# Optimization experiments

Hardware: AMD Instinct MI355X
Metric: run time of the kernel (lower is better)

## Reference

```python
import jax, jax.numpy as jnp
import numpy as np

B, C, H, W = 8, 256, 80, 80
NH, NP = 8, 4               # num_heads, num_points
CPH = C // NH               # channels per head


def conv1x1(x, w, b):
    # x: [B,Cin,H,W], w: [Cout,Cin], b: [Cout]
    return jnp.einsum('bchw,oc->bohw', x, w) + b[None, :, None, None]


def grid_sample_bilinear(img, grid):
    # img: [N,C,Hi,Wi], grid: [N,Hg,Wg,2] in [-1,1] (x,y), align_corners=True, zeros padding
    N, Cc, Hi, Wi = img.shape
    Hg, Wg = grid.shape[1], grid.shape[2]
    ix = (grid[..., 0] + 1.0) * 0.5 * (Wi - 1)
    iy = (grid[..., 1] + 1.0) * 0.5 * (Hi - 1)
    x0 = jnp.floor(ix); y0 = jnp.floor(iy)
    x1 = x0 + 1.0;      y1 = y0 + 1.0
    wx1 = ix - x0; wx0 = 1.0 - wx1
    wy1 = iy - y0; wy0 = 1.0 - wy1
    imf = img.reshape(N, Cc, Hi * Wi)

    def gather(xc, yc):
        valid = (xc >= 0) & (xc <= Wi - 1) & (yc >= 0) & (yc <= Hi - 1)
        xi = jnp.clip(xc, 0, Wi - 1).astype(jnp.int32)
        yi = jnp.clip(yc, 0, Hi - 1).astype(jnp.int32)
        idx = (yi * Wi + xi).reshape(N, 1, Hg * Wg)
        v = jnp.take_along_axis(imf, jnp.broadcast_to(idx, (N, Cc, Hg * Wg)), axis=2)
        v = v.reshape(N, Cc, Hg, Wg)
        return v * valid[:, None].astype(img.dtype)

    out = (gather(x0, y0) * (wx0 * wy0)[:, None]
           + gather(x1, y0) * (wx1 * wy0)[:, None]
           + gather(x0, y1) * (wx0 * wy1)[:, None]
           + gather(x1, y1) * (wx1 * wy1)[:, None])
    return out


def setup_inputs() -> dict:
    key = jax.random.key(0)
    ks = jax.random.split(key, 9)
    s = 1.0 / np.sqrt(C)
    x = jax.random.normal(ks[0], (B, C, H, W), dtype=jnp.float32)
    Wv = jax.random.normal(ks[1], (C, C), dtype=jnp.float32) * s
    bv = jnp.zeros((C,), dtype=jnp.float32)
    Woff = jax.random.normal(ks[2], (NH * NP * 2, C), dtype=jnp.float32) * 0.01
    boff = jax.random.normal(ks[3], (NH * NP * 2,), dtype=jnp.float32) * 0.01
    Wa = jax.random.normal(ks[4], (NH * NP, C), dtype=jnp.float32) * 0.01
    ba = jnp.full((NH * NP,), float(np.log(1.0 / NP)), dtype=jnp.float32)
    Wo = jax.random.normal(ks[5], (C, C), dtype=jnp.float32) * s
    bo = jnp.zeros((C,), dtype=jnp.float32)
    return {"x": x, "Wv": Wv, "bv": bv, "Woff": Woff, "boff": boff,
            "Wa": Wa, "ba": ba, "Wo": Wo, "bo": bo}


def reference(x, Wv, bv, Woff, boff, Wa, ba, Wo, bo):
    value = conv1x1(x, Wv, bv)                      # [B,C,H,W]
    offsets = conv1x1(x, Woff, boff)                # [B,NH*NP*2,H,W]
    attn = conv1x1(x, Wa, ba).reshape(B, NH, NP, H, W)
    attn = jax.nn.softmax(attn, axis=2)             # softmax over points

    gy, gx = jnp.meshgrid(jnp.linspace(-1.0, 1.0, H), jnp.linspace(-1.0, 1.0, W), indexing='ij')
    base_grid = jnp.stack((gx, gy), axis=-1)[None, None, None]          # [1,1,1,H,W,2]

    off = offsets.reshape(B, NH, NP, 2, H, W).transpose(0, 1, 2, 4, 5, 3)  # [B,NH,NP,H,W,2]
    grid = (base_grid + off).reshape(B * NH * NP, H, W, 2)

    v = value.reshape(B, NH, CPH, H, W)
    v = jnp.broadcast_to(v[:, :, None], (B, NH, NP, CPH, H, W)).reshape(B * NH * NP, CPH, H, W)

    sampled = grid_sample_bilinear(v, grid).reshape(B, NH, NP, CPH, H, W)
    weighted = (sampled * attn[:, :, :, None]).sum(axis=2)              # [B,NH,CPH,H,W]
    weighted = weighted.reshape(B, C, H, W)
    return conv1x1(weighted, Wo, bo) + x
```

## Files before the change

kernel.cpp:

```cpp
#include <hip/hip_runtime.h>
#include <cstddef>
#include <cstdint>

#define B_    8
#define C_    256
#define Himg  80
#define Wimg  80
#define HW_   6400
#define NH_   8
#define NP_   4
#define MPROJ 352

using bf16x8 = __attribute__((ext_vector_type(8))) short;
using f32x4  = __attribute__((ext_vector_type(4))) float;

__device__ __forceinline__ unsigned short f2bf(float f) {
    union { float f; uint32_t u; } v; v.f = f;
    uint32_t r = v.u + 0x7FFFu + ((v.u >> 16) & 1u);
    return (unsigned short)(r >> 16);
}
__device__ __forceinline__ float bf2f(unsigned short s) {
    union { uint32_t u; float f; } v; v.u = ((uint32_t)s) << 16;
    return v.f;
}

#define GLD16(gsrc, ldst) \
    __builtin_amdgcn_global_load_lds( \
        (const __attribute__((address_space(1))) unsigned int*)(gsrc), \
        (__attribute__((address_space(3))) unsigned int*)(ldst), 16, 0, 0)

__global__ __launch_bounds__(256) void prep_w(
        const float* __restrict__ Wv,  const float* __restrict__ bv,
        const float* __restrict__ Woff, const float* __restrict__ boff,
        const float* __restrict__ Wa,  const float* __restrict__ ba,
        const float* __restrict__ Wo,
        short* __restrict__ WcatBf, short* __restrict__ WoBf,
        float* __restrict__ bcat) {
    int o = blockIdx.x, t = threadIdx.x;
    if (o < 384) {
        const float* src = nullptr; float bias = 0.f;
        if (o < 256)      { src = Wv   + (size_t)o * 256;         bias = bv[o];         }
        else if (o < 320) { src = Woff + (size_t)(o - 256) * 256; bias = boff[o - 256]; }
        else if (o < 352) { src = Wa   + (size_t)(o - 320) * 256; bias = ba[o - 320];   }
        WcatBf[(size_t)o * 256 + t] = src ? (short)f2bf(src[t]) : (short)0;
        if (t == 0) bcat[o] = bias;
    } else {
        int oo = o - 384;
        WoBf[(size_t)oo * 256 + t] = (short)f2bf(Wo[(size_t)oo * 256 + t]);
    }
}

__global__ __launch_bounds__(256) void transpose_x(
        const float* __restrict__ x, short* __restrict__ xT) {
    __shared__ float tile[64][68];
    const int b = blockIdx.z, k0 = blockIdx.y * 64, p0 = blockIdx.x * 64;
    const int t = threadIdx.x;
    const float* xb = x + ((size_t)b * C_ + k0) * HW_ + p0;
    #pragma unroll
    for (int r = 0; r < 4; ++r) {
        int kk = r * 16 + (t >> 4);
        int pp = (t & 15) * 4;
        float4 v = *(const float4*)(xb + (size_t)kk * HW_ + pp);
        *(float4*)&tile[kk][pp] = v;
    }
    __syncthreads();
    const int pp = t >> 2, kc = (t & 3) * 16;
    short tmp[16];
    #pragma unroll
    for (int i = 0; i < 16; ++i) tmp[i] = (short)f2bf(tile[kc + i][pp]);
    short* dst = xT + ((size_t)b * HW_ + p0 + pp) * 256 + k0 + kc;
    *(bf16x8*)dst       = *(bf16x8*)tmp;
    *(bf16x8*)(dst + 8) = *(bf16x8*)(tmp + 8);
}

#define PSTAGE(buf, k0)                                                         \
    _Pragma("unroll")                                                           \
    for (int q = 0; q < 4; ++q) {                                               \
        int i = wid * 4 + q;                                                    \
        int row = i * 8 + (lane >> 3);                                          \
        int sc  = (lane & 7) ^ (row & 7);                                       \
        GLD16(Wb  + (size_t)(o0 + row) * 256 + (k0) + sc * 8,                   \
              &lA[(buf)][i * 512]);                                             \
        GLD16(xTb + (size_t)(p0 + row) * 256 + (k0) + sc * 8,                   \
              &lB[(buf)][i * 512]);                                             \
    }

#define PCOMPUTE(buf)                                                           \
    _Pragma("unroll")                                                           \
    for (int kk = 0; kk < 2; ++kk) {                                            \
        bf16x8 af[4], bfr[4];                                                   \
        _Pragma("unroll")                                                       \
        for (int m = 0; m < 4; ++m) {                                           \
            int row = wo0 + m * 16 + (lane & 15);                               \
            int cph = (kk * 4 + (lane >> 4)) ^ (row & 7);                       \
            af[m] = *(const bf16x8*)&lA[(buf)][row * 64 + cph * 8];             \
        }                                                                       \
        _Pragma("unroll")                                                       \
        for (int nn = 0; nn < 4; ++nn) {                                        \
            int row = wp0 + nn * 16 + (lane & 15);                              \
            int cph = (kk * 4 + (lane >> 4)) ^ (row & 7);                       \
            bfr[nn] = *(const bf16x8*)&lB[(buf)][row * 64 + cph * 8];           \
        }                                                                       \
        _Pragma("unroll")                                                       \
        for (int m = 0; m < 4; ++m)                                             \
            _Pragma("unroll")                                                   \
            for (int nn = 0; nn < 4; ++nn)                                      \
                acc[m][nn] = __builtin_amdgcn_mfma_f32_16x16x32_bf16(           \
                    af[m], bfr[nn], acc[m][nn], 0, 0, 0);                       \
    }

__global__ __launch_bounds__(256) void gemm_proj_mfma(
        const short* __restrict__ Wb, const float* __restrict__ bcat,
        const short* __restrict__ xT,
        short* __restrict__ val, float* __restrict__ meta) {
    __shared__ short lA[2][8192];
    __shared__ short lB[2][8192];
    const int n = blockIdx.x;
    const int w = (n & 7) * 150 + (n >> 3);
    const int b = w / 150;
    const int r150 = w % 150;
    const int o0 = (r150 / 50) * 128;
    const int p0 = (r150 % 50) * 128;
    const int t = threadIdx.x;
    const int wid = t >> 6, lane = t & 63;
    const int wo0 = (wid & 1) * 64, wp0 = (wid >> 1) * 64;
    const short* xTb = xT + (size_t)b * HW_ * 256;
    f32x4 acc[4][4] = {};

    PSTAGE(0, 0)
    __syncthreads();
    #pragma unroll
    for (int kt = 0; kt < 3; ++kt) {
        const int cur = kt & 1;
        PSTAGE(cur ^ 1, (kt + 1) * 64)
        PCOMPUTE(cur)
        __syncthreads();
    }
    PCOMPUTE(1)

    #pragma unroll
    for (int m = 0; m < 4; ++m) {
        int oc = o0 + wo0 + m * 16 + (lane >> 4) * 4;
        if (oc >= MPROJ) continue;
        float4 bias = *(const float4*)(bcat + oc);
        #pragma unroll
        for (int nn = 0; nn < 4; ++nn) {
            int p = p0 + wp0 + nn * 16 + (lane & 15);
            f32x4 a = acc[m][nn];
            float v0 = a[0] + bias.x, v1 = a[1] + bias.y;
            float v2 = a[2] + bias.z, v3 = a[3] + bias.w;
            if (oc < 256) {
                ushort4 u;
                u.x = f2bf(v0); u.y = f2bf(v1); u.z = f2bf(v2); u.w = f2bf(v3);
                *(ushort4*)(val + ((size_t)b * HW_ + p) * 256 + oc) = u;
            } else {
                float4 f; f.x = v0; f.y = v1; f.z = v2; f.w = v3;
                *(float4*)(meta + ((size_t)b * HW_ + p) * 96 + (oc - 256)) = f;
            }
        }
    }
}

__global__ __launch_bounds__(256) void sample_kern(
        const short* __restrict__ val, const float* __restrict__ meta,
        short* __restrict__ wout) {
    const int t = threadIdx.x;
    const int wid = t >> 6, lane = t & 63;
    const int sub = lane >> 5, li = lane & 31;
    const int h = li >> 2, j = li & 3;
    const int orig = blockIdx.x;
    const int b = orig & 7;
    const int p = (orig >> 3) * 8 + wid * 2 + sub;
    const int yy = p / Wimg;
    const int xx = p - yy * Wimg;

    const float* mrow = meta + ((size_t)b * HW_ + p) * 96;
    float4 lg = *(const float4*)(mrow + 64 + h * 4);
    float mx  = fmaxf(fmaxf(lg.x, lg.y), fmaxf(lg.z, lg.w));
    float e0 = __expf(lg.x - mx), e1 = __expf(lg.y - mx);
    float e2 = __expf(lg.z - mx), e3 = __expf(lg.w - mx);
    float inv = 1.f / (e0 + e1 + e2 + e3);
    float wgt[4] = {e0 * inv, e1 * inv, e2 * inv, e3 * inv};

    float4 offA = *(const float4*)(mrow + h * 8);
    float4 offB = *(const float4*)(mrow + h * 8 + 4);
    float ox[4] = {offA.x, offA.z, offB.x, offB.z};
    float oy[4] = {offA.y, offA.w, offB.y, offB.w};

    const short* vb = val + (size_t)b * HW_ * 256 + h * 32 + j * 8;

    float acc[8] = {};
    #pragma unroll
    for (int pt = 0; pt < NP_; ++pt) {
        float ix = (float)xx + ox[pt] * 39.5f;
        float iy = (float)yy + oy[pt] * 39.5f;
        float x0f = floorf(ix), y0f = floorf(iy);
        int   x0  = (int)x0f,   y0  = (int)y0f;
        float wx1 = ix - x0f, wx0 = 1.f - wx1;
        float wy1 = iy - y0f, wy0 = 1.f - wy1;
        int x0c = min(max(x0, 0), Wimg - 1), x1c = min(max(x0 + 1, 0), Wimg - 1);
        int y0c = min(max(y0, 0), Himg - 1), y1c = min(max(y0 + 1, 0), Himg - 1);
        float vx0 = (x0 >= 0 && x0 <= Wimg - 1)         ? wx0 : 0.f;
        float vx1 = (x0 + 1 >= 0 && x0 + 1 <= Wimg - 1) ? wx1 : 0.f;
        float vy0 = (y0 >= 0 && y0 <= Himg - 1)         ? wy0 : 0.f;
        float vy1 = (y0 + 1 >= 0 && y0 + 1 <= Himg - 1) ? wy1 : 0.f;
        bf16x8 u00 = *(const bf16x8*)(vb + (size_t)(y0c * Wimg + x0c) * 256);
        bf16x8 u01 = *(const bf16x8*)(vb + (size_t)(y0c * Wimg + x1c) * 256);
        bf16x8 u10 = *(const bf16x8*)(vb + (size_t)(y1c * Wimg + x0c) * 256);
        bf16x8 u11 = *(const bf16x8*)(vb + (size_t)(y1c * Wimg + x1c) * 256);
        float w00 = vy0 * vx0 * wgt[pt], w01 = vy0 * vx1 * wgt[pt];
        float w10 = vy1 * vx0 * wgt[pt], w11 = vy1 * vx1 * wgt[pt];
        #pragma unroll
        for (int c = 0; c < 8; ++c) {
            acc[c] += w00 * bf2f((unsigned short)u00[c])
                    + w01 * bf2f((unsigned short)u01[c])
                    + w10 * bf2f((unsigned short)u10[c])
                    + w11 * bf2f((unsigned short)u11[c]);
        }
    }
    short tmp[8];
    #pragma unroll
    for (int c = 0; c < 8; ++c) tmp[c] = (short)f2bf(acc[c]);
    *(bf16x8*)(wout + ((size_t)b * HW_ + p) * 256 + h * 32 + j * 8) = *(bf16x8*)tmp;
}

#define OSTAGE(buf, k0)                                                         \
    _Pragma("unroll")                                                           \
    for (int q = 0; q < 2; ++q) {                                               \
        int i = wid * 2 + q;                                                    \
        int row = i * 8 + (lane >> 3);                                          \
        int sc  = (lane & 7) ^ (row & 7);                                       \
        GLD16(Wb + (size_t)(o0 + row) * 256 + (k0) + sc * 8,                    \
              &lA[(buf)][i * 512]);                                             \
    }                                                                           \
    _Pragma("unroll")                                                           \
    for (int q = 0; q < 4; ++q) {                                               \
        int i = wid * 4 + q;                                                    \
        int row = i * 8 + (lane >> 3);                                          \
        int sc  = (lane & 7) ^ (row & 7);                                       \
        GLD16(wgtb + (size_t)(p0 + row) * 256 + (k0) + sc * 8,                  \
              &lB[(buf)][i * 512]);                                             \
    }

#define OCOMPUTE(buf)                                                           \
    _Pragma("unroll")                                                           \
    for (int kk = 0; kk < 2; ++kk) {                                            \
        bf16x8 af[4], bfr[2];                                                   \
        _Pragma("unroll")                                                       \
        for (int m = 0; m < 4; ++m) {                                           \
            int row = m * 16 + (lane & 15);                                     \
            int cph = (kk * 4 + (lane >> 4)) ^ (row & 7);                       \
            af[m] = *(const bf16x8*)&lA[(buf)][row * 64 + cph * 8];             \
        }                                                                       \
        _Pragma("unroll")                                                       \
        for (int nn = 0; nn < 2; ++nn) {                                        \
            int row = wid * 32 + nn * 16 + (lane & 15);                         \
            int cph = (kk * 4 + (lane >> 4)) ^ (row & 7);                       \
            bfr[nn] = *(const bf16x8*)&lB[(buf)][row * 64 + cph * 8];           \
        }                                                                       \
        _Pragma("unroll")                                                       \
        for (int m = 0; m < 4; ++m)                                             \
            _Pragma("unroll")                                                   \
            for (int nn = 0; nn < 2; ++nn)                                      \
                acc[m][nn] = __builtin_amdgcn_mfma_f32_16x16x32_bf16(           \
                    af[m], bfr[nn], acc[m][nn], 0, 0, 0);                       \
    }

__global__ __launch_bounds__(256) void gemm_out_mfma(
        const short* __restrict__ Wb, const float* __restrict__ bo,
        const short* __restrict__ wgt, const float* __restrict__ x,
        float* __restrict__ out) {
    __shared__ short lA[2][4096];
    __shared__ short lB[2][8192];
    const int n = blockIdx.x;
    const int w = (n & 7) * 200 + (n >> 3);
    const int b = w / 200;
    const int r200 = w % 200;
    const int o0 = (r200 / 50) * 64;
    const int p0 = (r200 % 50) * 128;
    const int t = threadIdx.x;
    const int wid = t >> 6, lane = t & 63;
    const short* wgtb = wgt + (size_t)b * HW_ * 256;
    f32x4 acc[4][2] = {};

    OSTAGE(0, 0)
    __syncthreads();
    #pragma unroll
    for (int kt = 0; kt < 3; ++kt) {
        const int cur = kt & 1;
        OSTAGE(cur ^ 1, (kt + 1) * 64)
        OCOMPUTE(cur)
        __syncthreads();
    }
    OCOMPUTE(1)

    #pragma unroll
    for (int m = 0; m < 4; ++m) {
        int oc = o0 + m * 16 + (lane >> 4) * 4;
        float4 bias = *(const float4*)(bo + oc);
        float br[4] = {bias.x, bias.y, bias.z, bias.w};
        #pragma unroll
        for (int nn = 0; nn < 2; ++nn) {
            int p = p0 + wid * 32 + nn * 16 + (lane & 15);
            f32x4 a = acc[m][nn];
            #pragma unroll
            for (int reg = 0; reg < 4; ++reg) {
                size_t ad = ((size_t)b * C_ + oc + reg) * HW_ + p;
                out[ad] = a[reg] + br[reg] + x[ad];
            }
        }
    }
}

extern "C" void kernel_launch(void* const* d_in, const int* in_sizes, int n_in,
                              void* d_out, int out_size, void* d_ws, size_t ws_size,
                              hipStream_t stream) {
    const float* x    = (const float*)d_in[0];
    const float* Wv   = (const float*)d_in[1];
    const float* bv   = (const float*)d_in[2];
    const float* Woff = (const float*)d_in[3];
    const float* boff = (const float*)d_in[4];
    const float* Wa   = (const float*)d_in[5];
    const float* ba   = (const float*)d_in[6];
    const float* Wo   = (const float*)d_in[7];
    const float* bo   = (const float*)d_in[8];
    float* out = (float*)d_out;
    char* base = (char*)d_ws;

    short* WcatBf = (short*)(base);
    short* WoBf   = (short*)(base + 196608);
    float* bcat   = (float*)(base + 327680);
    short* xT     = (short*)(base + 329728);
    short* val    = (short*)(base + 26544128);
    float* meta   = (float*)(base + 52758528);
    short* wbuf   = (short*)(base + 72419328);

    prep_w<<<dim3(640), dim3(256), 0, stream>>>(Wv, bv, Woff, boff, Wa, ba, Wo,
                                                WcatBf, WoBf, bcat);
    transpose_x<<<dim3(100, 4, 8), dim3(256), 0, stream>>>(x, xT);
    gemm_proj_mfma<<<dim3(1200), dim3(256), 0, stream>>>(WcatBf, bcat, xT, val, meta);
    sample_kern<<<dim3(6400), dim3(256), 0, stream>>>(val, meta, wbuf);
    gemm_out_mfma<<<dim3(1600), dim3(256), 0, stream>>>(WoBf, bo, wbuf, x, out);
}
```

Before: 109.4 us.

## Merge prep kernels, store value head-major, move softmax and offset scaling into projection epilogue

Merges the weight-conversion and x-transpose kernels into one launch, dispatched by block index. Changes the value tensor layout from pixel-major with 256 channels to head-major [B,NH,HW,32]. Each head's bilinear gathers now read a compact plane, which should improve cache locality. The projection GEMM epilogue now pre-scales offsets and computes the per-head softmax, which removes that work from the sampling kernel. The risks are scattered 8-byte stores in the GEMM epilogue and a bigger combined prep kernel.

```diff
diff --git a/kernel.cpp b/kernel.cpp
--- a/kernel.cpp
+++ b/kernel.cpp
@@ -29,32 +29,35 @@
         (const __attribute__((address_space(1))) unsigned int*)(gsrc), \
         (__attribute__((address_space(3))) unsigned int*)(ldst), 16, 0, 0)
 
-__global__ __launch_bounds__(256) void prep_w(
+__global__ __launch_bounds__(256) void prep_and_transpose(
         const float* __restrict__ Wv,  const float* __restrict__ bv,
         const float* __restrict__ Woff, const float* __restrict__ boff,
         const float* __restrict__ Wa,  const float* __restrict__ ba,
-        const float* __restrict__ Wo,
+        const float* __restrict__ Wo,  const float* __restrict__ x,
         short* __restrict__ WcatBf, short* __restrict__ WoBf,
-        float* __restrict__ bcat) {
-    int o = blockIdx.x, t = threadIdx.x;
-    if (o < 384) {
-        const float* src = nullptr; float bias = 0.f;
-        if (o < 256)      { src = Wv   + (size_t)o * 256;         bias = bv[o];         }
-        else if (o < 320) { src = Woff + (size_t)(o - 256) * 256; bias = boff[o - 256]; }
-        else if (o < 352) { src = Wa   + (size_t)(o - 320) * 256; bias = ba[o - 320];   }
-        WcatBf[(size_t)o * 256 + t] = src ? (short)f2bf(src[t]) : (short)0;
-        if (t == 0) bcat[o] = bias;
-    } else {
-        int oo = o - 384;
-        WoBf[(size_t)oo * 256 + t] = (short)f2bf(Wo[(size_t)oo * 256 + t]);
-    }
-}
-
-__global__ __launch_bounds__(256) void transpose_x(
-        const float* __restrict__ x, short* __restrict__ xT) {
+        float* __restrict__ bcat,   short* __restrict__ xT) {
     __shared__ float tile[64][68];
-    const int b = blockIdx.z, k0 = blockIdx.y * 64, p0 = blockIdx.x * 64;
+    const int bid = blockIdx.x;
     const int t = threadIdx.x;
+    if (bid < 640) {
+        int o = bid;
+        if (o < 384) {
+            const float* src = nullptr; float bias = 0.f;
+            if (o < 256)      { src = Wv   + (size_t)o * 256;         bias = bv[o];         }
+            else if (o < 320) { src = Woff + (size_t)(o - 256) * 256; bias = boff[o - 256]; }
+            else if (o < 352) { src = Wa   + (size_t)(o - 320) * 256; bias = ba[o - 320];   }
+            WcatBf[(size_t)o * 256 + t] = src ? (short)f2bf(src[t]) : (short)0;
+            if (t == 0) bcat[o] = bias;
+        } else {
+            int oo = o - 384;
+            WoBf[(size_t)oo * 256 + t] = (short)f2bf(Wo[(size_t)oo * 256 + t]);
+        }
+        return;
+    }
+    const int b2 = bid - 640;
+    const int p0 = (b2 % 100) * 64;
+    const int k0 = ((b2 / 100) & 3) * 64;
+    const int b  = b2 / 400;
     const float* xb = x + ((size_t)b * C_ + k0) * HW_ + p0;
     #pragma unroll
     for (int r = 0; r < 4; ++r) {
@@ -150,11 +153,22 @@
             float v0 = a[0] + bias.x, v1 = a[1] + bias.y;
             float v2 = a[2] + bias.z, v3 = a[3] + bias.w;
             if (oc < 256) {
+                int h = oc >> 5, c0 = oc & 31;
                 ushort4 u;
                 u.x = f2bf(v0); u.y = f2bf(v1); u.z = f2bf(v2); u.w = f2bf(v3);
-                *(ushort4*)(val + ((size_t)b * HW_ + p) * 256 + oc) = u;
+                *(ushort4*)(val + (((size_t)(b * NH_ + h) * HW_) + p) * 32 + c0) = u;
+            } else if (oc < 320) {
+                float4 f;
+                f.x = v0 * 39.5f; f.y = v1 * 39.5f;
+                f.z = v2 * 39.5f; f.w = v3 * 39.5f;
+                *(float4*)(meta + ((size_t)b * HW_ + p) * 96 + (oc - 256)) = f;
             } else {
-                float4 f; f.x = v0; f.y = v1; f.z = v2; f.w = v3;
+                float mx = fmaxf(fmaxf(v0, v1), fmaxf(v2, v3));
+                float e0 = __expf(v0 - mx), e1 = __expf(v1 - mx);
+                float e2 = __expf(v2 - mx), e3 = __expf(v3 - mx);
+                float inv = 1.f / (e0 + e1 + e2 + e3);
+                float4 f;
+                f.x = e0 * inv; f.y = e1 * inv; f.z = e2 * inv; f.w = e3 * inv;
                 *(float4*)(meta + ((size_t)b * HW_ + p) * 96 + (oc - 256)) = f;
             }
         }
@@ -175,25 +189,21 @@
     const int xx = p - yy * Wimg;
 
     const float* mrow = meta + ((size_t)b * HW_ + p) * 96;
-    float4 lg = *(const float4*)(mrow + 64 + h * 4);
-    float mx  = fmaxf(fmaxf(lg.x, lg.y), fmaxf(lg.z, lg.w));
-    float e0 = __expf(lg.x - mx), e1 = __expf(lg.y - mx);
-    float e2 = __expf(lg.z - mx), e3 = __expf(lg.w - mx);
-    float inv = 1.f / (e0 + e1 + e2 + e3);
-    float wgt[4] = {e0 * inv, e1 * inv, e2 * inv, e3 * inv};
+    float4 wv = *(const float4*)(mrow + 64 + h * 4);
+    float wgt[4] = {wv.x, wv.y, wv.z, wv.w};
 
     float4 offA = *(const float4*)(mrow + h * 8);
     float4 offB = *(const float4*)(mrow + h * 8 + 4);
     float ox[4] = {offA.x, offA.z, offB.x, offB.z};
     float oy[4] = {offA.y, offA.w, offB.y, offB.w};
 
-    const short* vb = val + (size_t)b * HW_ * 256 + h * 32 + j * 8;
+    const short* vb = val + ((size_t)(b * NH_ + h) * HW_) * 32 + j * 8;
 
     float acc[8] = {};
     #pragma unroll
     for (int pt = 0; pt < NP_; ++pt) {
-        float ix = (float)xx + ox[pt] * 39.5f;
-        float iy = (float)yy + oy[pt] * 39.5f;
+        float ix = (float)xx + ox[pt];
+        float iy = (float)yy + oy[pt];
         float x0f = floorf(ix), y0f = floorf(iy);
         int   x0  = (int)x0f,   y0  = (int)y0f;
         float wx1 = ix - x0f, wx0 = 1.f - wx1;
@@ -204,10 +214,10 @@
         float vx1 = (x0 + 1 >= 0 && x0 + 1 <= Wimg - 1) ? wx1 : 0.f;
         float vy0 = (y0 >= 0 && y0 <= Himg - 1)         ? wy0 : 0.f;
         float vy1 = (y0 + 1 >= 0 && y0 + 1 <= Himg - 1) ? wy1 : 0.f;
-        bf16x8 u00 = *(const bf16x8*)(vb + (size_t)(y0c * Wimg + x0c) * 256);
-        bf16x8 u01 = *(const bf16x8*)(vb + (size_t)(y0c * Wimg + x1c) * 256);
-        bf16x8 u10 = *(const bf16x8*)(vb + (size_t)(y1c * Wimg + x0c) * 256);
-        bf16x8 u11 = *(const bf16x8*)(vb + (size_t)(y1c * Wimg + x1c) * 256);
+        bf16x8 u00 = *(const bf16x8*)(vb + (size_t)(y0c * Wimg + x0c) * 32);
+        bf16x8 u01 = *(const bf16x8*)(vb + (size_t)(y0c * Wimg + x1c) * 32);
+        bf16x8 u10 = *(const bf16x8*)(vb + (size_t)(y1c * Wimg + x0c) * 32);
+        bf16x8 u11 = *(const bf16x8*)(vb + (size_t)(y1c * Wimg + x1c) * 32);
         float w00 = vy0 * vx0 * wgt[pt], w01 = vy0 * vx1 * wgt[pt];
         float w10 = vy1 * vx0 * wgt[pt], w11 = vy1 * vx1 * wgt[pt];
         #pragma unroll
@@ -335,9 +345,8 @@
     float* meta   = (float*)(base + 52758528);
     short* wbuf   = (short*)(base + 72419328);
 
-    prep_w<<<dim3(640), dim3(256), 0, stream>>>(Wv, bv, Woff, boff, Wa, ba, Wo,
-                                                WcatBf, WoBf, bcat);
-    transpose_x<<<dim3(100, 4, 8), dim3(256), 0, stream>>>(x, xT);
+    prep_and_transpose<<<dim3(3840), dim3(256), 0, stream>>>(
+        Wv, bv, Woff, boff, Wa, ba, Wo, x, WcatBf, WoBf, bcat, xT);
     gemm_proj_mfma<<<dim3(1200), dim3(256), 0, stream>>>(WcatBf, bcat, xT, val, meta);
     sample_kern<<<dim3(6400), dim3(256), 0, stream>>>(val, meta, wbuf);
     gemm_out_mfma<<<dim3(1600), dim3(256), 0, stream>>>(WoBf, bo, wbuf, x, out);
```

Result: faster. 100.9 us (-7.8%).
